# Performance work log

Measured on AMD Instinct MI355X. Metric: run time of the kernel, lower is better.

## Reference

```python
import jax, jax.numpy as jnp
import numpy as np

B, T, P = 2, 6, 20480
DIM, DIM_STATIC, IN_HRES, EMB_HRES = 96, 8, 28, 32
G0, G1 = 3, 10
HEADDIM, D_STATE, D_CONV = 16, 1, 3
D_INNER = DIM + EMB_HRES            # expand = 1 -> 128
NHEADS = D_INNER // HEADDIM         # 8
CONV_DIM = D_INNER + 2 * D_STATE    # 130 (ngroups = 1)
D_IN_PROJ = 2 * D_INNER + 2 * D_STATE + NHEADS  # 266
EPS = 1e-5


def _ln(x):
    # LayerNorm without affine (elementwise_affine=False)
    mu = jnp.mean(x, -1, keepdims=True)
    var = jnp.mean((x - mu) ** 2, -1, keepdims=True)
    return (x - mu) * jax.lax.rsqrt(var + EPS)


def _wpart(x):
    # window_partition, order='spatial_first'
    b, t, p, c = x.shape
    x = x.reshape(b, t // G0, G0, p // G1, G1, c).transpose(0, 1, 3, 2, 4, 5)
    return x.reshape(-1, G0 * G1, c)


def _wrev(w, b, t, p):
    # window_reverse, order='spatial_first' (translated verbatim from the torch code)
    c = w.shape[-1]
    x = w.reshape(b, p // G1, t // G0, G1, G0, c).transpose(0, 3, 1, 4, 2, 5)
    return x.reshape(b, t, p, c)


def _mamba2(u, conv_w, conv_b, dt_bias, A_log, Dp, norm_w):
    # Mamba2 core with in_proj/out_proj hoisted outside (as in RiverMamba).
    # u: (N, L, D_IN_PROJ) -> (N, L, D_INNER)
    n, L, _ = u.shape
    z = u[..., :D_INNER]
    xBC = u[..., D_INNER:D_INNER + CONV_DIM]
    dt = jax.nn.softplus(u[..., D_INNER + CONV_DIM:] + dt_bias)  # (n,L,H)
    # causal depthwise conv along L
    xp = jnp.pad(xBC, ((0, 0), (D_CONV - 1, 0), (0, 0)))
    xBC = sum(xp[:, k:k + L, :] * conv_w[:, k] for k in range(D_CONV)) + conv_b
    xBC = jax.nn.silu(xBC)
    xh = xBC[..., :D_INNER].reshape(n, L, NHEADS, HEADDIM)
    Bm = xBC[..., D_INNER:D_INNER + D_STATE]   # (n,L,S)  ngroups=1 -> broadcast over heads
    Cm = xBC[..., D_INNER + D_STATE:]          # (n,L,S)
    A = -jnp.exp(A_log)                        # (H,)
    dA = jnp.exp(dt * A)                       # (n,L,H)
    dBx = dt[..., None, None] * xh[..., None] * Bm[:, :, None, None, :]  # (n,L,H,Hd,S)

    def step(h, inp):
        dA_t, dBx_t, C_t = inp
        h = h * dA_t[:, :, None, None] + dBx_t
        y = jnp.einsum('nhps,ns->nhp', h, C_t)
        return h, y

    h0 = jnp.zeros((n, NHEADS, HEADDIM, D_STATE), u.dtype)
    _, ys = jax.lax.scan(step, h0, (jnp.swapaxes(dA, 0, 1), jnp.swapaxes(dBx, 0, 1), jnp.swapaxes(Cm, 0, 1)))
    y = jnp.swapaxes(ys, 0, 1) + xh * Dp[None, None, :, None]   # D skip
    # RMSNormGated (norm_before_gate=False): gate first, then rmsnorm
    y = y.reshape(n, L, D_INNER) * jax.nn.silu(z)
    y = y * jax.lax.rsqrt(jnp.mean(y * y, -1, keepdims=True) + EPS) * norm_w
    return y


def _forward(x, x_static, x_hres, x_curves, embed_w, embed_b, loan1_w, loan1_b, loan2_w, loan2_b,
             in_proj_w, conv_w_f, conv_b_f, dt_bias_f, A_log_f, D_f, norm_w_f,
             conv_w_b, conv_b_b, dt_bias_b, A_log_b, D_b, norm_w_b,
             out_proj_w, mlp_w1, mlp_b1, mlp_w2, mlp_b2):
    curve = x_curves[:, 0, 0, :]                       # (B,P) curve_id=0
    gat = jax.vmap(lambda a, c: a[:, c, :])            # serialization
    x = gat(x, curve)
    xs = gat(x_static, curve)
    xh = gat(x_hres, curve)
    # --- part 1 ---
    hr = jnp.tanh(xh @ embed_w + embed_b)              # InputEmbed
    xc = jnp.concatenate([x, hr], -1)                  # (B,T,P,128)
    xn = _ln(xc) + jnp.tanh(xs @ loan1_w + loan1_b)    # norm1 + LOAN1
    u = xn @ in_proj_w                                 # (B,T,P,266)
    u_b = _wpart(jnp.flip(u, axis=2))                  # backward direction (flip points)
    u_f = _wpart(u)
    y_f = _wrev(_mamba2(u_f, conv_w_f, conv_b_f, dt_bias_f, A_log_f, D_f, norm_w_f), B, T, P)
    y_b = _wrev(_mamba2(u_b, conv_w_b, conv_b_b, dt_bias_b, A_log_b, D_b, norm_w_b), B, T, P)
    y = 0.5 * (y_f + jnp.flip(y_b, axis=2))            # is_divide_out=True
    x1 = x + y @ out_proj_w                            # residual 1
    # --- part 2 ---
    z = _ln(x1) + jnp.tanh(xs @ loan2_w + loan2_b)     # norm2 + LOAN2
    z = jax.nn.gelu(z @ mlp_w1 + mlp_b1, approximate=False) @ mlp_w2 + mlp_b2
    return x1 + z                                      # residual 2


def setup_inputs() -> dict:
    key = jax.random.key(0)
    ks = jax.random.split(key, 40)
    idx = iter(range(40))

    def nrm(shape, s):
        return jax.random.normal(ks[next(idx)], shape, jnp.float32) * s

    inp = {}
    inp['x'] = nrm((B, T, P, DIM), 1.0)
    inp['x_static'] = nrm((B, T, P, DIM_STATIC), 1.0)
    inp['x_hres'] = nrm((B, T, P, IN_HRES), 1.0)
    perms = jnp.stack([jax.random.permutation(ks[next(idx)], P) for _ in range(B)])
    inp['x_curves'] = perms.reshape(B, 1, 1, P).astype(jnp.int32)
    inp['embed_w'] = nrm((IN_HRES, EMB_HRES), 0.1)
    inp['embed_b'] = jnp.zeros(EMB_HRES, jnp.float32)
    inp['loan1_w'] = nrm((DIM_STATIC, D_INNER), 0.1)
    inp['loan1_b'] = jnp.zeros(D_INNER, jnp.float32)
    inp['loan2_w'] = nrm((DIM_STATIC, DIM), 0.1)
    inp['loan2_b'] = jnp.zeros(DIM, jnp.float32)
    inp['in_proj_w'] = nrm((D_INNER, D_IN_PROJ), 0.05)
    for sfx in ('f', 'b'):
        inp['conv_w_' + sfx] = nrm((CONV_DIM, D_CONV), 0.2)
        inp['conv_b_' + sfx] = jnp.zeros(CONV_DIM, jnp.float32)
        inp['dt_bias_' + sfx] = jnp.full((NHEADS,), -2.25, jnp.float32)  # softplus^-1(0.1)
        inp['A_log_' + sfx] = jnp.log(jax.random.uniform(ks[next(idx)], (NHEADS,), jnp.float32, 1.0, 16.0))
        inp['D_' + sfx] = jnp.ones(NHEADS, jnp.float32)
        inp['norm_w_' + sfx] = jnp.ones(D_INNER, jnp.float32)
    inp['out_proj_w'] = nrm((D_INNER, DIM), 0.05)
    inp['mlp_w1'] = nrm((DIM, DIM), 0.05)
    inp['mlp_b1'] = jnp.zeros(DIM, jnp.float32)
    inp['mlp_w2'] = nrm((DIM, DIM), 0.05)
    inp['mlp_b2'] = jnp.zeros(DIM, jnp.float32)
    return inp


def reference(x, x_static, x_hres, x_curves, embed_w, embed_b, loan1_w, loan1_b, loan2_w, loan2_b,
              in_proj_w, conv_w_f, conv_b_f, dt_bias_f, A_log_f, D_f, norm_w_f,
              conv_w_b, conv_b_b, dt_bias_b, A_log_b, D_b, norm_w_b,
              out_proj_w, mlp_w1, mlp_b1, mlp_w2, mlp_b2):
    return _forward(x, x_static, x_hres, x_curves, embed_w, embed_b, loan1_w, loan1_b, loan2_w, loan2_b,
                    in_proj_w, conv_w_f, conv_b_f, dt_bias_f, A_log_f, D_f, norm_w_f,
                    conv_w_b, conv_b_b, dt_bias_b, A_log_b, D_b, norm_w_b,
                    out_proj_w, mlp_w1, mlp_b1, mlp_w2, mlp_b2)
```

## Files before the change

kernel.cpp:

```cpp
#include <hip/hip_runtime.h>
#include <math.h>

typedef __attribute__((ext_vector_type(8))) short short8;
typedef __attribute__((ext_vector_type(4))) float f32x4;
typedef __attribute__((ext_vector_type(4))) unsigned int u32x4;

#define BB 2
#define TT 6
#define PP 20480
#define EPSc 1e-5f

#define WS_WIN   0u
#define WS_WOF   69632u
#define WS_WOB   94208u
#define WS_W1    118784u
#define WS_W2    137216u
#define WS_EW    155648u
#define WS_L1    157696u
#define WS_L2    165888u
#define WS_INV   172032u
#define WS_XN    335872u
#define WS_YF    63250432u
#define WS_YB    126164992u

__device__ __forceinline__ float asf(unsigned int u){ float f; __builtin_memcpy(&f, &u, 4); return f; }
__device__ __forceinline__ unsigned short f2bf(float f){
  unsigned int u; __builtin_memcpy(&u, &f, 4);
  unsigned int r = (u + 0x7fffu + ((u >> 16) & 1u)) >> 16;
  return (unsigned short)r;
}
__device__ __forceinline__ float fast_sigm(float x){ return __builtin_amdgcn_rcpf(1.0f + __expf(-x)); }
__device__ __forceinline__ float fast_tanh(float x){ return 1.0f - 2.0f * __builtin_amdgcn_rcpf(1.0f + __expf(2.0f * x)); }
__device__ __forceinline__ float fast_gelu(float v){
  float s = v * 0.70710678118654752f;
  float ax = fabsf(s);
  float t = __builtin_amdgcn_rcpf(1.0f + 0.3275911f * ax);
  float p = t * (0.254829592f + t * (-0.284496736f + t * (1.421413741f + t * (-1.453152027f + t * 1.061405429f))));
  float er = 1.0f - p * __expf(-ax * ax);
  er = (s < 0.0f) ? -er : er;
  return 0.5f * v * (1.0f + er);
}

__global__ __launch_bounds__(256) void k0_wprep(
    const float* __restrict__ win, const float* __restrict__ wout,
    const float* __restrict__ w1m, const float* __restrict__ w2m,
    const float* __restrict__ nwf, const float* __restrict__ nwb,
    const float* __restrict__ ew, const float* __restrict__ eb,
    const float* __restrict__ l1w, const float* __restrict__ l1b,
    const float* __restrict__ l2w, const float* __restrict__ l2b,
    unsigned char* __restrict__ ws)
{
  int gt = blockIdx.x * 256 + threadIdx.x;
  int g = gt >> 6, lane = gt & 63;
  int ln = lane & 15, kg = lane >> 4;
  union { unsigned short u[8]; short8 s; } cv;
  unsigned int dst; int gl;
  if (g < 68){
    gl = g; int nt = gl >> 2, kk = gl & 3;
    int n = nt * 16 + ln;
    #pragma unroll
    for (int j = 0; j < 8; j++){
      int k = kk * 32 + kg * 8 + j;
      cv.u[j] = f2bf((n < 266) ? win[(size_t)k * 266 + n] : 0.0f);
    }
    dst = WS_WIN;
  } else if (g < 116){
    int isb = (g >= 92); gl = g - (isb ? 92 : 68);
    int nt = gl >> 2, kk = gl & 3;
    int n = nt * 16 + ln;
    const float* nw = isb ? nwb : nwf;
    #pragma unroll
    for (int j = 0; j < 8; j++){
      int k = kk * 32 + kg * 8 + j;
      cv.u[j] = f2bf(0.5f * nw[k] * wout[(size_t)k * 96 + n]);
    }
    dst = isb ? WS_WOB : WS_WOF;
  } else if (g < 152){
    int is2 = (g >= 134); gl = g - (is2 ? 134 : 116);
    int nt = gl / 3, kk = gl % 3;
    int n = nt * 16 + ln;
    const float* src = is2 ? w2m : w1m;
    #pragma unroll
    for (int j = 0; j < 8; j++){
      int k = kk * 32 + kg * 8 + j;
      cv.u[j] = f2bf(src[(size_t)k * 96 + n]);
    }
    dst = is2 ? WS_W2 : WS_W1;
  } else if (g < 154){
    gl = g - 152; int n = gl * 16 + ln;
    #pragma unroll
    for (int j = 0; j < 8; j++){
      int k = kg * 8 + j;
      float f = (k < 28) ? ew[k * 32 + n] : ((k == 28) ? eb[n] : 0.0f);
      cv.u[j] = f2bf(f);
    }
    dst = WS_EW;
  } else if (g < 162){
    gl = g - 154; int n = gl * 16 + ln;
    #pragma unroll
    for (int j = 0; j < 8; j++){
      int k = kg * 8 + j;
      float f = (k < 8) ? l1w[k * 128 + n] : ((k == 8) ? l1b[n] : 0.0f);
      cv.u[j] = f2bf(f);
    }
    dst = WS_L1;
  } else {
    gl = g - 162; int n = gl * 16 + ln;
    #pragma unroll
    for (int j = 0; j < 8; j++){
      int k = kg * 8 + j;
      float f = (k < 8) ? l2w[k * 96 + n] : ((k == 8) ? l2b[n] : 0.0f);
      cv.u[j] = f2bf(f);
    }
    dst = WS_L2;
  }
  *(short8*)(ws + dst + (size_t)(gl * 64 + lane) * 16) = cv.s;
}

__global__ __launch_bounds__(256) void k0b_inv(
    const int* __restrict__ curves, unsigned char* __restrict__ ws)
{
  int i = blockIdx.x * 256 + threadIdx.x;
  int p = i % PP;
  ((int*)(ws + WS_INV))[(i / PP) * PP + curves[i]] = p;
}

__global__ __launch_bounds__(256) void k1_prep(
    const float* __restrict__ x, const float* __restrict__ xst,
    const float* __restrict__ xhr, unsigned char* __restrict__ ws)
{
  __shared__ unsigned short hrl[4][16][40];
  __shared__ unsigned short lol[4][16][136];
  int tid = threadIdx.x, lane = tid & 63, w = tid >> 6;
  int pos0 = blockIdx.x * 64;
  int b = pos0 / (TT * PP); int r = pos0 % (TT * PP);
  int t = r / PP; int c0 = r % PP;
  size_t tbase = (size_t)(b * TT + t) * PP;

  {
    int arow = w * 16 + (lane & 15);
    int g = lane >> 4;
    const float* hrow = xhr + (tbase + c0 + arow) * 28;
    float4 f0 = *(const float4*)(hrow + g * 8);
    float4 f1 = (g < 3) ? *(const float4*)(hrow + g * 8 + 4) : (float4){0.f,0.f,0.f,0.f};
    const float4* xsr = (const float4*)(xst + (tbase + c0 + arow) * 8);
    float4 s0 = xsr[0], s1 = xsr[1];
    union { unsigned short u[8]; short8 s; } ae, al;
    ae.u[0]=f2bf(f0.x); ae.u[1]=f2bf(f0.y); ae.u[2]=f2bf(f0.z); ae.u[3]=f2bf(f0.w);
    ae.u[4]=f2bf(f1.x); ae.u[5]=f2bf(f1.y); ae.u[6]=f2bf(f1.z); ae.u[7]=f2bf(f1.w);
    if (g == 3){ ae.u[4] = 0x3F80u; ae.u[5]=0; ae.u[6]=0; ae.u[7]=0; }
    #pragma unroll
    for (int j = 0; j < 8; j++) al.u[j] = 0;
    if (g == 0){
      al.u[0]=f2bf(s0.x); al.u[1]=f2bf(s0.y); al.u[2]=f2bf(s0.z); al.u[3]=f2bf(s0.w);
      al.u[4]=f2bf(s1.x); al.u[5]=f2bf(s1.y); al.u[6]=f2bf(s1.z); al.u[7]=f2bf(s1.w);
    } else if (g == 1){ al.u[0] = 0x3F80u; }
    const short8* BE = (const short8*)(ws + WS_EW);
    const short8* BL = (const short8*)(ws + WS_L1);
    f32x4 he0 = {0.f,0.f,0.f,0.f}, he1 = {0.f,0.f,0.f,0.f};
    he0 = __builtin_amdgcn_mfma_f32_16x16x32_bf16(ae.s, BE[lane], he0, 0, 0, 0);
    he1 = __builtin_amdgcn_mfma_f32_16x16x32_bf16(ae.s, BE[64 + lane], he1, 0, 0, 0);
    f32x4 lo[8];
    #pragma unroll
    for (int nt = 0; nt < 8; nt++){
      f32x4 z = {0.f,0.f,0.f,0.f};
      lo[nt] = __builtin_amdgcn_mfma_f32_16x16x32_bf16(al.s, BL[nt * 64 + lane], z, 0, 0, 0);
    }
    int rl = (lane >> 4) * 4, col = lane & 15;
    #pragma unroll
    for (int r2 = 0; r2 < 4; r2++){
      hrl[w][rl + r2][col]      = f2bf(fast_tanh(he0[r2]));
      hrl[w][rl + r2][16 + col] = f2bf(fast_tanh(he1[r2]));
    }
    #pragma unroll
    for (int nt = 0; nt < 8; nt++){
      #pragma unroll
      for (int r2 = 0; r2 < 4; r2++)
        lol[w][rl + r2][nt * 16 + col] = f2bf(fast_tanh(lo[nt][r2]));
    }
  }
  __syncthreads();

  int pp = tid >> 2, q = tid & 3;
  int c = c0 + pp;
  union { float4 v4[8]; float v[32]; } xv;
  if (q < 3){
    const float4* xr4 = (const float4*)(x + (tbase + c) * 96 + q * 32);
    #pragma unroll
    for (int j = 0; j < 8; j++) xv.v4[j] = xr4[j];
  } else {
    const u32x4* hp = (const u32x4*)(&hrl[pp >> 4][pp & 15][0]);
    #pragma unroll
    for (int j = 0; j < 4; j++){
      u32x4 hv = hp[j];
      #pragma unroll
      for (int e = 0; e < 4; e++){
        unsigned int u = hv[e];
        xv.v[j*8 + e*2]     = asf(u << 16);
        xv.v[j*8 + e*2 + 1] = asf(u & 0xffff0000u);
      }
    }
  }
  float s = 0.f, s2 = 0.f;
  #pragma unroll
  for (int j = 0; j < 32; j++){ float v = xv.v[j]; s += v; s2 += v * v; }
  s += __shfl_xor(s, 1); s2 += __shfl_xor(s2, 1);
  s += __shfl_xor(s, 2); s2 += __shfl_xor(s2, 2);
  float mu = s * (1.0f / 128.0f);
  float rs = __builtin_amdgcn_rsqf(s2 * (1.0f / 128.0f) - mu * mu + EPSc);

  int p = ((const int*)(ws + WS_INV))[b * PP + c];
  const u32x4* lp = (const u32x4*)(&lol[pp >> 4][pp & 15][q * 32]);
  u32x4* dst = (u32x4*)((unsigned short*)(ws + WS_XN) + (tbase + p) * 128 + q * 32);
  #pragma unroll
  for (int j = 0; j < 4; j++){
    u32x4 lv = lp[j];
    unsigned int pk[4];
    #pragma unroll
    for (int e = 0; e < 4; e++){
      unsigned int lu = lv[e];
      float l0 = asf(lu << 16), l1 = asf(lu & 0xffff0000u);
      int idx = j*8 + e*2;
      float r0 = (xv.v[idx]   - mu) * rs + l0;
      float r1 = (xv.v[idx+1] - mu) * rs + l1;
      asm("v_cvt_pk_bf16_f32 %0, %1, %2" : "=v"(pk[e]) : "v"(r0), "v"(r1));
    }
    u32x4 stv = { pk[0], pk[1], pk[2], pk[3] };
    dst[j] = stv;
  }
}

__global__ __launch_bounds__(256, 4) void k2_mamba(
    unsigned char* __restrict__ ws,
    const float* __restrict__ cwf, const float* __restrict__ cbf,
    const float* __restrict__ dtbf, const float* __restrict__ alf,
    const float* __restrict__ Dpf,
    const float* __restrict__ cwb, const float* __restrict__ cbb,
    const float* __restrict__ dtbb, const float* __restrict__ alb,
    const float* __restrict__ Dpb)
{
  __shared__ unsigned short uld[2][30][272];
  int blk = blockIdx.x;
  int b = blk >> 11; int tb = (blk >> 10) & 1; int pbh = blk & 1023;
  int wid = threadIdx.x >> 6, lane = threadIdx.x & 63;
  int pairIdx = wid >> 1, dir = wid & 1;
  int pb = pbh * 2 + pairIdx;

  const unsigned short* xn = (const unsigned short*)(ws + WS_XN);
  int lr = dir * 16 + (lane & 15); if (lr > 29) lr = 29;
  int g0r = lr / 10, g1r = lr - g0r * 10;
  const unsigned short* arow = xn + (((size_t)(b * TT + tb * 3 + g0r) * PP) + (size_t)pb * 10 + g1r) * 128 + (lane >> 4) * 8;
  short8 afr[4];
  #pragma unroll
  for (int kk = 0; kk < 4; kk++) afr[kk] = *(const short8*)(arow + kk * 32);
  const short8* bbm = (const short8*)(ws + WS_WIN);
  int row0 = dir * 16 + (lane >> 4) * 4;
  int col0 = lane & 15;
  #pragma unroll
  for (int half = 0; half < 2; half++){
    const int n0 = half ? 9 : 0;
    const int cnt = half ? 8 : 9;
    f32x4 acc[9];
    #pragma unroll
    for (int i = 0; i < 9; i++) acc[i] = (f32x4){0.f,0.f,0.f,0.f};
    #pragma unroll
    for (int kk = 0; kk < 4; kk++){
      #pragma unroll
      for (int j = 0; j < 9; j++){
        if (j < cnt){
          short8 bf = bbm[((n0 + j) * 4 + kk) * 64 + lane];
          acc[j] = __builtin_amdgcn_mfma_f32_16x16x32_bf16(afr[kk], bf, acc[j], 0, 0, 0);
        }
      }
    }
    #pragma unroll
    for (int j = 0; j < 9; j++){
      if (j < cnt){
        int col = (n0 + j) * 16 + col0;
        #pragma unroll
        for (int r2 = 0; r2 < 4; r2++){
          int row = row0 + r2;
          if (row < 30 && col < 266) uld[pairIdx][row][col] = f2bf(acc[j][r2]);
        }
      }
    }
  }
  __syncthreads();

  const float* cw  = dir ? cwb  : cwf;
  const float* cb  = dir ? cbb  : cbf;
  const float* dtb = dir ? dtbb : dtbf;
  const float* al  = dir ? alb  : alf;
  const float* Dp  = dir ? Dpb  : Dpf;
  unsigned int* ybuf = (unsigned int*)(ws + (dir ? WS_YB : WS_YF));
  int pbown = dir ? (2047 - pb) : pb;
  int cbase = (tb * 1024 + (pbown >> 1)) * 6 + (pbown & 1);
  unsigned int wbase = (unsigned int)b * 7864320u + (unsigned int)lane;

  int c0 = lane * 2;
  int hh = lane >> 3;
  float w00=cw[c0*3+0], w01=cw[c0*3+1], w02=cw[c0*3+2], cb0=cb[c0];
  float w10=cw[c0*3+3], w11=cw[c0*3+4], w12=cw[c0*3+5], cb1=cb[c0+1];
  float wB0=cw[128*3+0], wB1=cw[128*3+1], wB2=cw[128*3+2], cbB=cb[128];
  float wC0=cw[129*3+0], wC1=cw[129*3+1], wC2=cw[129*3+2], cbC=cb[129];
  float Ah = -__expf(al[hh]);
  float dtbh = dtb[hh], Dh = Dp[hh];
  const unsigned short* tile = &uld[pairIdx][0][0];

  float xp10=0,xp20=0,xp11=0,xp21=0, Bp1=0,Bp2=0, Cp1=0,Cp2=0;
  float h0=0.f, h1=0.f;
  #pragma unroll
  for (int l = 0; l < 30; l++){
    const int Kl = (l/3)*12288 + (l%3)*2;
    const int Kd = Kl / 20480, Km = Kl % 20480;
    const int urow_b = (l/10)*10 + 9 - (l%10);
    const unsigned short* ur = tile + (dir ? urow_b : l) * 272;
    unsigned int zz = *(const unsigned int*)(ur + c0);
    unsigned int xx = *(const unsigned int*)(ur + 128 + c0);
    unsigned int bcw = *(const unsigned int*)(ur + 256);
    float dtr = asf((unsigned int)ur[258 + hh] << 16);
    float z0 = asf(zz << 16), z1 = asf(zz & 0xffff0000u);
    float xr0 = asf(xx << 16), xr1 = asf(xx & 0xffff0000u);
    float Br = asf(bcw << 16), Cr = asf(bcw & 0xffff0000u);
    float xc0 = fmaf(w02, xr0, fmaf(w01, xp10, fmaf(w00, xp20, cb0)));
    float xc1 = fmaf(w12, xr1, fmaf(w11, xp11, fmaf(w10, xp21, cb1)));
    float Bc  = fmaf(wB2, Br, fmaf(wB1, Bp1, fmaf(wB0, Bp2, cbB)));
    float Cc  = fmaf(wC2, Cr, fmaf(wC1, Cp1, fmaf(wC0, Cp2, cbC)));
    xp20=xp10; xp10=xr0; xp21=xp11; xp11=xr1;
    Bp2=Bp1; Bp1=Br; Cp2=Cp1; Cp1=Cr;
    float xh0 = xc0 * fast_sigm(xc0), xh1 = xc1 * fast_sigm(xc1);
    float Bv = Bc * fast_sigm(Bc), Cv = Cc * fast_sigm(Cc);
    float dtx = dtr + dtbh;
    float e = __expf(-fabsf(dtx));
    float dt = fmaxf(dtx, 0.0f) + __logf(1.0f + e);
    float dA = __expf(dt * Ah);
    float sB = dt * Bv;
    h0 = fmaf(h0, dA, xh0 * sB);
    h1 = fmaf(h1, dA, xh1 * sB);
    float y0 = fmaf(h0, Cv, xh0 * Dh) * (z0 * fast_sigm(z0));
    float y1 = fmaf(h1, Cv, xh1 * Dh) * (z1 * fast_sigm(z1));
    unsigned int pk;
    asm("v_cvt_pk_bf16_f32 %0, %1, %2" : "=v"(pk) : "v"(y0), "v"(y1));
    int pD = Km + cbase, tD = Kd;
    if (pD >= 20480){ pD -= 20480; tD++; }
    if (dir) pD = 20479 - pD;
    ybuf[wbase + (unsigned int)tD * 1310720u + (unsigned int)pD * 64u] = pk;
  }
}

__global__ __launch_bounds__(256) void k3_epi(
    const unsigned char* __restrict__ ws,
    const float* __restrict__ x, const float* __restrict__ xst,
    const int* __restrict__ curves,
    const float* __restrict__ b1, const float* __restrict__ b2,
    float* __restrict__ out)
{
  __shared__ unsigned short Abuf[2][64 * 128];
  int tid = threadIdx.x; int lane = tid & 63; int w = tid >> 6;
  int pos0 = blockIdx.x * 64;
  int b = pos0 / (TT * PP); int rm = pos0 % (TT * PP);
  int t = rm / PP; int p0 = rm % PP;
  size_t tbase = (size_t)(b * TT + t) * PP;
  const int* cur = curves + b * PP;
  unsigned char* b0 = (unsigned char*)(&Abuf[0][0]);
  unsigned char* b1p = (unsigned char*)(&Abuf[1][0]);

  int colA = lane & 15, ag = lane >> 4;
  int crow0 = w * 16 + ag * 4;

  float xres[6][4];
  #pragma unroll
  for (int r2 = 0; r2 < 4; r2++){
    int cp = cur[p0 + crow0 + r2];
    const float* xr = x + (tbase + cp) * 96;
    #pragma unroll
    for (int nt = 0; nt < 6; nt++) xres[nt][r2] = xr[nt * 16 + colA];
  }
  union { unsigned short u[8]; short8 s; } al;
  {
    int arow = w * 16 + colA;
    int cpa = cur[p0 + arow];
    const float4* xsr = (const float4*)(xst + (tbase + cpa) * 8);
    float4 s0 = xsr[0], s1 = xsr[1];
    #pragma unroll
    for (int j = 0; j < 8; j++) al.u[j] = 0;
    if (ag == 0){
      al.u[0]=f2bf(s0.x); al.u[1]=f2bf(s0.y); al.u[2]=f2bf(s0.z); al.u[3]=f2bf(s0.w);
      al.u[4]=f2bf(s1.x); al.u[5]=f2bf(s1.y); al.u[6]=f2bf(s1.z); al.u[7]=f2bf(s1.w);
    } else if (ag == 1){ al.u[0] = 0x3F80u; }
  }

  {
    int pp = tid >> 2, q = tid & 3;
    const u32x4* yfp = (const u32x4*)(ws + WS_YF) + (size_t)(pos0 + pp) * 16 + q * 4;
    const u32x4* ybp = (const u32x4*)(ws + WS_YB) + (size_t)(pos0 + pp) * 16 + q * 4;
    u32x4 fv[4], bv[4];
    #pragma unroll
    for (int j = 0; j < 4; j++){ fv[j] = yfp[j]; bv[j] = ybp[j]; }
    float ssf = 0.f, ssb = 0.f;
    #pragma unroll
    for (int j = 0; j < 4; j++){
      #pragma unroll
      for (int e = 0; e < 4; e++){
        unsigned int uf = fv[j][e], ub = bv[j][e];
        float a0 = asf(uf << 16), a1 = asf(uf & 0xffff0000u);
        float c0v = asf(ub << 16), c1v = asf(ub & 0xffff0000u);
        ssf += a0*a0 + a1*a1; ssb += c0v*c0v + c1v*c1v;
      }
    }
    ssf += __shfl_xor(ssf, 1); ssb += __shfl_xor(ssb, 1);
    ssf += __shfl_xor(ssf, 2); ssb += __shfl_xor(ssb, 2);
    float rf = __builtin_amdgcn_rsqf(ssf * (1.0f/128.0f) + EPSc);
    float rb = __builtin_amdgcn_rsqf(ssb * (1.0f/128.0f) + EPSc);
    #pragma unroll
    for (int j = 0; j < 4; j++){
      unsigned int pkf[4], pkb[4];
      #pragma unroll
      for (int e = 0; e < 4; e++){
        unsigned int uf = fv[j][e], ub = bv[j][e];
        float a0 = asf(uf << 16) * rf, a1 = asf(uf & 0xffff0000u) * rf;
        float c0v = asf(ub << 16) * rb, c1v = asf(ub & 0xffff0000u) * rb;
        asm("v_cvt_pk_bf16_f32 %0, %1, %2" : "=v"(pkf[e]) : "v"(a0), "v"(a1));
        asm("v_cvt_pk_bf16_f32 %0, %1, %2" : "=v"(pkb[e]) : "v"(c0v), "v"(c1v));
      }
      int off = pp * 256 + ((q * 64 + j * 16) ^ ((pp & 7) << 4));
      u32x4 sf = { pkf[0], pkf[1], pkf[2], pkf[3] };
      u32x4 sb = { pkb[0], pkb[1], pkb[2], pkb[3] };
      *(u32x4*)(b0 + off) = sf;
      *(u32x4*)(b1p + off) = sb;
    }
  }
  __syncthreads();

  f32x4 acc[6], accl[6];
  #pragma unroll
  for (int i = 0; i < 6; i++){ acc[i] = (f32x4){0.f,0.f,0.f,0.f}; accl[i] = (f32x4){0.f,0.f,0.f,0.f}; }
  {
    int arow = w * 16 + colA;
    unsigned int rmask = (unsigned int)((arow & 7) << 4);
    const short8* WF = (const short8*)(ws + WS_WOF);
    const short8* WB = (const short8*)(ws + WS_WOB);
    #pragma unroll
    for (int kk = 0; kk < 4; kk++){
      int offc = arow * 256 + (int)(((unsigned)(kk * 64 + ag * 16)) ^ rmask);
      short8 aff = *(const short8*)(b0 + offc);
      short8 abb = *(const short8*)(b1p + offc);
      #pragma unroll
      for (int nt = 0; nt < 6; nt++){
        acc[nt] = __builtin_amdgcn_mfma_f32_16x16x32_bf16(aff, WF[(nt*4+kk)*64 + lane], acc[nt], 0, 0, 0);
        acc[nt] = __builtin_amdgcn_mfma_f32_16x16x32_bf16(abb, WB[(nt*4+kk)*64 + lane], acc[nt], 0, 0, 0);
      }
    }
    const short8* WL = (const short8*)(ws + WS_L2);
    #pragma unroll
    for (int nt = 0; nt < 6; nt++)
      accl[nt] = __builtin_amdgcn_mfma_f32_16x16x32_bf16(al.s, WL[nt*64 + lane], accl[nt], 0, 0, 0);
  }
  float X1[6][4];
  #pragma unroll
  for (int nt = 0; nt < 6; nt++)
    #pragma unroll
    for (int r2 = 0; r2 < 4; r2++) X1[nt][r2] = acc[nt][r2] + xres[nt][r2];
  float mu[4], rsv[4];
  {
    float sA[4], sQ[4];
    #pragma unroll
    for (int r2 = 0; r2 < 4; r2++){
      float s = 0.f, s2 = 0.f;
      #pragma unroll
      for (int nt = 0; nt < 6; nt++){ float v = X1[nt][r2]; s += v; s2 += v * v; }
      sA[r2] = s; sQ[r2] = s2;
    }
    #pragma unroll
    for (int m = 1; m < 16; m <<= 1){
      #pragma unroll
      for (int r2 = 0; r2 < 4; r2++){ sA[r2] += __shfl_xor(sA[r2], m); sQ[r2] += __shfl_xor(sQ[r2], m); }
    }
    #pragma unroll
    for (int r2 = 0; r2 < 4; r2++){
      mu[r2] = sA[r2] * (1.0f / 96.0f);
      rsv[r2] = __builtin_amdgcn_rsqf(sQ[r2] * (1.0f / 96.0f) - mu[r2] * mu[r2] + EPSc);
    }
  }
  __syncthreads();
  #pragma unroll
  for (int nt = 0; nt < 6; nt++){
    #pragma unroll
    for (int r2 = 0; r2 < 4; r2++){
      float tv = (X1[nt][r2] - mu[r2]) * rsv[r2] + fast_tanh(accl[nt][r2]);
      int crow = crow0 + r2, n = nt * 16 + colA;
      *(unsigned short*)(b0 + crow * 256 + ((n * 2) ^ ((crow & 7) << 4))) = f2bf(tv);
    }
  }
  __syncthreads();

  f32x4 acc2[6];
  #pragma unroll
  for (int i = 0; i < 6; i++) acc2[i] = (f32x4){0.f,0.f,0.f,0.f};
  {
    int arow = w * 16 + colA;
    unsigned int rmask = (unsigned int)((arow & 7) << 4);
    const short8* W1f = (const short8*)(ws + WS_W1);
    #pragma unroll
    for (int kk = 0; kk < 3; kk++){
      int offc = arow * 256 + (int)(((unsigned)(kk * 64 + ag * 16)) ^ rmask);
      short8 af = *(const short8*)(b0 + offc);
      #pragma unroll
      for (int nt = 0; nt < 6; nt++)
        acc2[nt] = __builtin_amdgcn_mfma_f32_16x16x32_bf16(af, W1f[(nt*3+kk)*64 + lane], acc2[nt], 0, 0, 0);
    }
  }
  float ge[6][4];
  #pragma unroll
  for (int nt = 0; nt < 6; nt++){
    float bv = b1[nt * 16 + colA];
    #pragma unroll
    for (int r2 = 0; r2 < 4; r2++) ge[nt][r2] = fast_gelu(acc2[nt][r2] + bv);
  }
  __syncthreads();
  #pragma unroll
  for (int nt = 0; nt < 6; nt++){
    #pragma unroll
    for (int r2 = 0; r2 < 4; r2++){
      int crow = crow0 + r2, n = nt * 16 + colA;
      *(unsigned short*)(b0 + crow * 256 + ((n * 2) ^ ((crow & 7) << 4))) = f2bf(ge[nt][r2]);
    }
  }
  __syncthreads();

  f32x4 acc3[6];
  #pragma unroll
  for (int i = 0; i < 6; i++) acc3[i] = (f32x4){0.f,0.f,0.f,0.f};
  {
    int arow = w * 16 + colA;
    unsigned int rmask = (unsigned int)((arow & 7) << 4);
    const short8* W2f = (const short8*)(ws + WS_W2);
    #pragma unroll
    for (int kk = 0; kk < 3; kk++){
      int offc = arow * 256 + (int)(((unsigned)(kk * 64 + ag * 16)) ^ rmask);
      short8 af = *(const short8*)(b0 + offc);
      #pragma unroll
      for (int nt = 0; nt < 6; nt++)
        acc3[nt] = __builtin_amdgcn_mfma_f32_16x16x32_bf16(af, W2f[(nt*3+kk)*64 + lane], acc3[nt], 0, 0, 0);
    }
  }
  #pragma unroll
  for (int r2 = 0; r2 < 4; r2++){
    int crow = crow0 + r2;
    size_t ob = (tbase + p0 + crow) * 96;
    #pragma unroll
    for (int nt = 0; nt < 6; nt++){
      int n = nt * 16 + colA;
      out[ob + n] = acc3[nt][r2] + b2[n] + X1[nt][r2];
    }
  }
}

extern "C" void kernel_launch(void* const* d_in, const int* in_sizes, int n_in,
                              void* d_out, int out_size, void* d_ws, size_t ws_size,
                              hipStream_t stream)
{
  const float* x     = (const float*)d_in[0];
  const float* xst   = (const float*)d_in[1];
  const float* xhr   = (const float*)d_in[2];
  const int*   curves= (const int*)d_in[3];
  const float* embw  = (const float*)d_in[4];
  const float* embb  = (const float*)d_in[5];
  const float* l1w   = (const float*)d_in[6];
  const float* l1b   = (const float*)d_in[7];
  const float* l2w   = (const float*)d_in[8];
  const float* l2b   = (const float*)d_in[9];
  const float* winp  = (const float*)d_in[10];
  const float* cwf   = (const float*)d_in[11];
  const float* cbf   = (const float*)d_in[12];
  const float* dtbf  = (const float*)d_in[13];
  const float* alf   = (const float*)d_in[14];
  const float* Df    = (const float*)d_in[15];
  const float* nwf   = (const float*)d_in[16];
  const float* cwb   = (const float*)d_in[17];
  const float* cbb   = (const float*)d_in[18];
  const float* dtbb  = (const float*)d_in[19];
  const float* alb   = (const float*)d_in[20];
  const float* Db    = (const float*)d_in[21];
  const float* nwb   = (const float*)d_in[22];
  const float* wout  = (const float*)d_in[23];
  const float* w1    = (const float*)d_in[24];
  const float* b1    = (const float*)d_in[25];
  const float* w2    = (const float*)d_in[26];
  const float* b2    = (const float*)d_in[27];
  unsigned char* ws  = (unsigned char*)d_ws;

  k0_wprep<<<42, 256, 0, stream>>>(winp, wout, w1, w2, nwf, nwb,
                                   embw, embb, l1w, l1b, l2w, l2b, ws);
  k0b_inv<<<160, 256, 0, stream>>>(curves, ws);
  k1_prep<<<3840, 256, 0, stream>>>(x, xst, xhr, ws);
  k2_mamba<<<4096, 256, 0, stream>>>(ws, cwf, cbf, dtbf, alf, Df,
                                         cwb, cbb, dtbb, alb, Db);
  k3_epi<<<3840, 256, 0, stream>>>(ws, x, xst, curves, b1, b2, (float*)d_out);
}
```

Baseline: 455.4 us.

## Precompute per-head dt/dA/B/C gates lane-parallel and broadcast via cross-lane ops

The per-step softplus, exp and SiLU for the B, C and dt channels were previously computed redundantly by every lane for every step of the scan. They are now computed once per (step, head) across the wavefront, with each lane handling one step/head combination in 4 chunks. The scan loop fetches these values with ds_bpermute and readlane. The LDS row stride is also padded from 272 to 276 to reduce bank conflicts. The trade-off is extra cross-lane permute traffic inside the serial loop in exchange for fewer transcendental operations per step.

```diff
diff --git a/kernel.cpp b/kernel.cpp
--- a/kernel.cpp
+++ b/kernel.cpp
@@ -24,6 +24,7 @@
 #define WS_YB    126164992u
 
 __device__ __forceinline__ float asf(unsigned int u){ float f; __builtin_memcpy(&f, &u, 4); return f; }
+__device__ __forceinline__ int f2i(float f){ int i; __builtin_memcpy(&i, &f, 4); return i; }
 __device__ __forceinline__ unsigned short f2bf(float f){
   unsigned int u; __builtin_memcpy(&u, &f, 4);
   unsigned int r = (u + 0x7fffu + ((u >> 16) & 1u)) >> 16;
@@ -230,6 +231,13 @@
   }
 }
 
+__device__ __forceinline__ int urow_of(int s, int dir){
+  int g0 = (s >= 20) ? 2 : ((s >= 10) ? 1 : 0);
+  int g1 = s - g0 * 10;
+  return dir ? (g0 * 10 + 9 - g1) : s;
+}
+
+#define ULDS 276
 __global__ __launch_bounds__(256, 4) void k2_mamba(
     unsigned char* __restrict__ ws,
     const float* __restrict__ cwf, const float* __restrict__ cbf,
@@ -239,7 +247,7 @@
     const float* __restrict__ dtbb, const float* __restrict__ alb,
     const float* __restrict__ Dpb)
 {
-  __shared__ unsigned short uld[2][30][272];
+  __shared__ unsigned short uld[2][30][ULDS];
   int blk = blockIdx.x;
   int b = blk >> 11; int tb = (blk >> 10) & 1; int pbh = blk & 1023;
   int wid = threadIdx.x >> 6, lane = threadIdx.x & 63;
@@ -296,6 +304,7 @@
   int pbown = dir ? (2047 - pb) : pb;
   int cbase = (tb * 1024 + (pbown >> 1)) * 6 + (pbown & 1);
   unsigned int wbase = (unsigned int)b * 7864320u + (unsigned int)lane;
+  const unsigned short* tile = &uld[pairIdx][0][0];
 
   int c0 = lane * 2;
   int hh = lane >> 3;
@@ -303,38 +312,61 @@
   float w10=cw[c0*3+3], w11=cw[c0*3+4], w12=cw[c0*3+5], cb1=cb[c0+1];
   float wB0=cw[128*3+0], wB1=cw[128*3+1], wB2=cw[128*3+2], cbB=cb[128];
   float wC0=cw[129*3+0], wC1=cw[129*3+1], wC2=cw[129*3+2], cbC=cb[129];
-  float Ah = -__expf(al[hh]);
-  float dtbh = dtb[hh], Dh = Dp[hh];
-  const unsigned short* tile = &uld[pairIdx][0][0];
-
-  float xp10=0,xp20=0,xp11=0,xp21=0, Bp1=0,Bp2=0, Cp1=0,Cp2=0;
+  float Dh = Dp[hh];
+
+  float dAc[4], sBc[4], Cvc[4];
+  {
+    int h2 = lane & 7;
+    int lrow = lane >> 3;
+    float dtb2 = dtb[h2];
+    float Ah2 = -__expf(al[h2]);
+    #pragma unroll
+    for (int cci = 0; cci < 4; cci++){
+      int l = cci * 8 + lrow; if (l > 29) l = 29;
+      float Braw[3], Craw[3];
+      #pragma unroll
+      for (int tap = 0; tap < 3; tap++){
+        int sp = l - tap;
+        if (sp >= 0){
+          unsigned int wv = *(const unsigned int*)(tile + urow_of(sp, dir) * ULDS + 256);
+          Braw[tap] = asf(wv << 16);
+          Craw[tap] = asf(wv & 0xffff0000u);
+        } else { Braw[tap] = 0.f; Craw[tap] = 0.f; }
+      }
+      float Bcc = fmaf(wB2, Braw[0], fmaf(wB1, Braw[1], fmaf(wB0, Braw[2], cbB)));
+      float Ccc = fmaf(wC2, Craw[0], fmaf(wC1, Craw[1], fmaf(wC0, Craw[2], cbC)));
+      float Bvv = Bcc * fast_sigm(Bcc);
+      Cvc[cci]  = Ccc * fast_sigm(Ccc);
+      float dtr = asf((unsigned int)tile[urow_of(l, dir) * ULDS + 258 + h2] << 16);
+      float dtx = dtr + dtb2;
+      float e = __expf(-fabsf(dtx));
+      float dt = fmaxf(dtx, 0.0f) + __logf(1.0f + e);
+      dAc[cci] = __expf(dt * Ah2);
+      sBc[cci] = dt * Bvv;
+    }
+  }
+
+  int vbase = (lane >> 3) << 2;
+  float xp10=0,xp20=0,xp11=0,xp21=0;
   float h0=0.f, h1=0.f;
   #pragma unroll
   for (int l = 0; l < 30; l++){
     const int Kl = (l/3)*12288 + (l%3)*2;
     const int Kd = Kl / 20480, Km = Kl % 20480;
     const int urow_b = (l/10)*10 + 9 - (l%10);
-    const unsigned short* ur = tile + (dir ? urow_b : l) * 272;
+    const unsigned short* ur = tile + (dir ? urow_b : l) * ULDS;
     unsigned int zz = *(const unsigned int*)(ur + c0);
     unsigned int xx = *(const unsigned int*)(ur + 128 + c0);
-    unsigned int bcw = *(const unsigned int*)(ur + 256);
-    float dtr = asf((unsigned int)ur[258 + hh] << 16);
+    const int chn = l >> 3, rrl = l & 7;
+    float dA = asf((unsigned int)__builtin_amdgcn_ds_bpermute(vbase + (rrl << 5), f2i(dAc[chn])));
+    float sB = asf((unsigned int)__builtin_amdgcn_ds_bpermute(vbase + (rrl << 5), f2i(sBc[chn])));
+    float Cv = asf((unsigned int)__builtin_amdgcn_readlane(f2i(Cvc[chn]), rrl * 8));
     float z0 = asf(zz << 16), z1 = asf(zz & 0xffff0000u);
     float xr0 = asf(xx << 16), xr1 = asf(xx & 0xffff0000u);
-    float Br = asf(bcw << 16), Cr = asf(bcw & 0xffff0000u);
     float xc0 = fmaf(w02, xr0, fmaf(w01, xp10, fmaf(w00, xp20, cb0)));
     float xc1 = fmaf(w12, xr1, fmaf(w11, xp11, fmaf(w10, xp21, cb1)));
-    float Bc  = fmaf(wB2, Br, fmaf(wB1, Bp1, fmaf(wB0, Bp2, cbB)));
-    float Cc  = fmaf(wC2, Cr, fmaf(wC1, Cp1, fmaf(wC0, Cp2, cbC)));
     xp20=xp10; xp10=xr0; xp21=xp11; xp11=xr1;
-    Bp2=Bp1; Bp1=Br; Cp2=Cp1; Cp1=Cr;
     float xh0 = xc0 * fast_sigm(xc0), xh1 = xc1 * fast_sigm(xc1);
-    float Bv = Bc * fast_sigm(Bc), Cv = Cc * fast_sigm(Cc);
-    float dtx = dtr + dtbh;
-    float e = __expf(-fabsf(dtx));
-    float dt = fmaxf(dtx, 0.0f) + __logf(1.0f + e);
-    float dA = __expf(dt * Ah);
-    float sB = dt * Bv;
     h0 = fmaf(h0, dA, xh0 * sB);
     h1 = fmaf(h1, dA, xh1 * sB);
     float y0 = fmaf(h0, Cv, xh0 * Dh) * (z0 * fast_sigm(z0));
```

After: 432.2 us. -5.1%, faster.
